# Kernel tuning notes

Hardware: AMD Instinct MI355X
Metric: run time of the kernel (lower is better)

The kernel has to match this reference:

```python
import jax, jax.numpy as jnp
import numpy as np

N_NODES = 40000
N_EDGES = 640000
D_FEAT = 128
HIDDEN = 128
N_GRAPHS = 512


def setup_inputs() -> dict:
    key = jax.random.key(0)
    ks = jax.random.split(key, 6)
    x = jax.random.normal(ks[0], (N_NODES, D_FEAT), dtype=jnp.float32)
    edge_index = jax.random.randint(ks[1], (2, N_EDGES), 0, N_NODES, dtype=jnp.int32)
    batch = jnp.sort(jax.random.randint(ks[2], (N_NODES,), 0, N_GRAPHS, dtype=jnp.int32))
    s1 = 1.0 / np.sqrt(D_FEAT)
    s2 = 1.0 / np.sqrt(HIDDEN)
    W1 = jax.random.normal(ks[3], (D_FEAT, HIDDEN), dtype=jnp.float32) * s1
    b1 = jnp.zeros((HIDDEN,), dtype=jnp.float32)
    W2 = jax.random.normal(ks[4], (HIDDEN, HIDDEN), dtype=jnp.float32) * s2
    b2 = jnp.zeros((HIDDEN,), dtype=jnp.float32)
    Wfc = jax.random.normal(ks[5], (HIDDEN, 1), dtype=jnp.float32) * s2
    bfc = jnp.zeros((1,), dtype=jnp.float32)
    return {"x": x, "edge_index": edge_index, "batch": batch,
            "W1": W1, "b1": b1, "W2": W2, "b2": b2, "Wfc": Wfc, "bfc": bfc}


def _gcn_conv(x, edge_index, W, b):
    # PyG GCNConv: linear transform, add self-loops, symmetric deg^{-1/2} norm,
    # scatter-add messages from row (source) to col (target), then bias.
    n = x.shape[0]
    h = x @ W  # [N, H]
    row, col = edge_index[0], edge_index[1]
    ones = jnp.ones_like(col, dtype=h.dtype)
    deg = 1.0 + jax.ops.segment_sum(ones, col, num_segments=n)  # self-loop included
    dinv = jax.lax.rsqrt(deg)  # [N]
    norm = dinv[row] * dinv[col]  # [E]
    msg = h[row] * norm[:, None]  # [E, H]
    out = jax.ops.segment_sum(msg, col, num_segments=n)
    out = out + h * (dinv * dinv)[:, None]  # self-loop contribution
    return out + b


def _mean_pool(x, batch, num_graphs):
    sums = jax.ops.segment_sum(x, batch, num_segments=num_graphs)
    cnt = jax.ops.segment_sum(jnp.ones((x.shape[0],), dtype=x.dtype), batch, num_segments=num_graphs)
    return sums / jnp.maximum(cnt, 1.0)[:, None]


def reference(x, edge_index, batch, W1, b1, W2, b2, Wfc, bfc):
    h = jax.nn.relu(_gcn_conv(x, edge_index, W1, b1))
    h = jax.nn.relu(_gcn_conv(h, edge_index, W2, b2))
    g = _mean_pool(h, batch, N_GRAPHS)  # [G, H]
    return g @ Wfc + bfc  # [G, 1]
```

## Files before the change

kernel.cpp:

```cpp
#include <hip/hip_runtime.h>
#include <hip/hip_fp16.h>

#define N_NODES 40000
#define N_EDGES 640000
#define NFEAT   128
#define N_GRAPHS 512
#define SCAN_NB 157
#define NBKT    157
#define BKT_CAP 8192
#define BIN_BLK_EDGES 2048
#define NBLK_A ((N_EDGES + BIN_BLK_EDGES - 1) / BIN_BLK_EDGES)
#define EPAD_MAX (N_EDGES + 3 * N_NODES)

__global__ void init_misc_kernel(int* __restrict__ gcursor, int* __restrict__ gcnt,
                                 float* __restrict__ out, const float* __restrict__ bfc,
                                 __half* __restrict__ hsent) {
    int t = threadIdx.x;
    if (t < NBKT) gcursor[t] = 0;
    float b = bfc[0];
    for (int i = t; i < N_GRAPHS; i += 256) { gcnt[i] = 0; out[i] = b; }
    if (t < NFEAT) hsent[t] = __float2half(0.0f);
}

__global__ void batch_hist_kernel(const int* __restrict__ batch, int* __restrict__ gcnt, int n) {
    int i = blockIdx.x * blockDim.x + threadIdx.x;
    if (i < n) atomicAdd(&gcnt[batch[i]], 1);
}

__global__ __launch_bounds__(256) void bin_kernel(const int* __restrict__ ei,
                                                  int* __restrict__ gcursor,
                                                  unsigned int* __restrict__ binned) {
    __shared__ int lhist[NBKT];
    __shared__ int lbase[NBKT];
    const int t  = threadIdx.x;
    const int e0 = blockIdx.x * BIN_BLK_EDGES;

    if (t < NBKT) lhist[t] = 0;
    __syncthreads();

    int creg[BIN_BLK_EDGES / 256];
    #pragma unroll
    for (int i = 0; i < BIN_BLK_EDGES / 256; ++i) {
        int e = e0 + i * 256 + t;
        creg[i] = (e < N_EDGES) ? ei[N_EDGES + e] : -1;
        if (creg[i] >= 0) atomicAdd(&lhist[creg[i] >> 8], 1);
    }
    __syncthreads();

    if (t < NBKT) { lbase[t] = atomicAdd(&gcursor[t], lhist[t]); lhist[t] = 0; }
    __syncthreads();

    #pragma unroll
    for (int i = 0; i < BIN_BLK_EDGES / 256; ++i) {
        int c = creg[i];
        if (c >= 0) {
            int e = e0 + i * 256 + t;
            int r = ei[e];
            int bkt = c >> 8;
            int slot = atomicAdd(&lhist[bkt], 1);
            binned[(size_t)bkt * BKT_CAP + lbase[bkt] + slot] =
                (unsigned int)r | ((unsigned int)(c & 255) << 16);
        }
    }
}

__global__ __launch_bounds__(256) void bucket_hist_kernel(const unsigned int* __restrict__ binned,
                                                          const int* __restrict__ gcursor,
                                                          float* __restrict__ dinv,
                                                          int* __restrict__ rowptr,
                                                          int* __restrict__ bsums) {
    __shared__ int chist[256];
    __shared__ int scn[256];
    const int b = blockIdx.x, t = threadIdx.x;
    chist[t] = 0;
    __syncthreads();
    const int cnt = gcursor[b];
    const unsigned int* src = binned + (size_t)b * BKT_CAP;
    for (int i = t; i < cnt; i += 256) atomicAdd(&chist[src[i] >> 16], 1);
    __syncthreads();
    const int col = b * 256 + t;
    const int valid = (col < N_NODES);
    int d = chist[t];
    if (valid) dinv[col] = rsqrtf(1.0f + (float)d);
    int pd = valid ? ((d + 3) & ~3) : 0;
    scn[t] = pd;
    __syncthreads();
    for (int off = 1; off < 256; off <<= 1) {
        int add = (t >= off) ? scn[t - off] : 0;
        __syncthreads();
        scn[t] += add;
        __syncthreads();
    }
    if (valid) rowptr[col] = scn[t] - pd;
    if (t == 255) bsums[b] = scn[255];
}

__global__ void scan157_kernel(int* __restrict__ bsums, int* __restrict__ rowptr) {
    __shared__ int tmp[256];
    int t = threadIdx.x;
    int v = (t < NBKT) ? bsums[t] : 0;
    tmp[t] = v;
    __syncthreads();
    for (int off = 1; off < 256; off <<= 1) {
        int add = (t >= off) ? tmp[t - off] : 0;
        __syncthreads();
        tmp[t] += add;
        __syncthreads();
    }
    if (t < NBKT) bsums[t] = tmp[t] - v;
    if (t == 255) rowptr[N_NODES] = tmp[255];
}

template <typename IdxT>
__global__ __launch_bounds__(256) void bucket_scatter_kernel(const unsigned int* __restrict__ binned,
                                                             const int* __restrict__ gcursor,
                                                             const int* __restrict__ bsums,
                                                             int* __restrict__ rowptr,
                                                             IdxT* __restrict__ csr) {
    __shared__ int ccur[256];
    const int b = blockIdx.x, t = threadIdx.x;
    const int col = b * 256 + t;
    const int base = bsums[b];
    int startp = 0;
    if (col < N_NODES) {
        startp = rowptr[col] + base;
        rowptr[col] = startp;
    }
    ccur[t] = startp;
    __syncthreads();
    const int cnt = gcursor[b];
    const unsigned int* src = binned + (size_t)b * BKT_CAP;
    for (int i = t; i < cnt; i += 256) {
        unsigned int u = src[i];
        int slot = atomicAdd(&ccur[u >> 16], 1);
        csr[slot] = (IdxT)(u & 0xFFFFu);
    }
    __syncthreads();
    if (col < N_NODES) {
        int cur = ccur[t];
        int deg = cur - startp;
        int endp = startp + ((deg + 3) & ~3);
        for (int p = cur; p < endp; ++p) csr[p] = (IdxT)N_NODES;
    }
}

__device__ inline float4 load_h4(const __half* p) {
    uint2 raw = *(const uint2*)p;
    __half2 h0 = *(__half2*)&raw.x;
    __half2 h1 = *(__half2*)&raw.y;
    float2 f0 = __half22float2(h0);
    float2 f1 = __half22float2(h1);
    return make_float4(f0.x, f0.y, f1.x, f1.y);
}
__device__ inline float4 load4v(const float* p)  { return *(const float4*)(p); }
__device__ inline float4 load4v(const __half* p) { return load_h4(p); }

template <typename InT>
__global__ __launch_bounds__(256, 4) void gemm64h_kernel(const InT* __restrict__ X,
                                                         const float* __restrict__ W,
                                                         const float* __restrict__ dinv,
                                                         __half* __restrict__ H) {
    __shared__ float Ws[128 * 64];
    const int colhalf = blockIdx.x & 1;
    const int tile    = blockIdx.x >> 1;

    for (int i = threadIdx.x; i < 2048; i += 256) {
        int k   = i >> 4;
        int cc4 = (i & 15) * 4;
        *(float4*)(Ws + k * 64 + cc4) = *(const float4*)(W + k * 128 + colhalf * 64 + cc4);
    }
    __syncthreads();

    const int rg = threadIdx.x >> 4;
    const int cg = threadIdx.x & 15;
    const int row0 = tile * 64 + rg * 4;
    const InT* x0 = X + (size_t)row0 * NFEAT;

    float acc[4][4] = {};
    float4 xc[4], xn[4];
    #pragma unroll
    for (int i = 0; i < 4; i++) xc[i] = load4v(x0 + (size_t)i * NFEAT);

    #pragma unroll 4
    for (int k = 0; k < 128; k += 4) {
        const int kn = (k + 4) & 127;
        #pragma unroll
        for (int i = 0; i < 4; i++) xn[i] = load4v(x0 + (size_t)i * NFEAT + kn);

        float4 wv[4];
        #pragma unroll
        for (int m = 0; m < 4; m++) wv[m] = *(const float4*)(Ws + (k + m) * 64 + cg * 4);

        #pragma unroll
        for (int i = 0; i < 4; i++) {
            const float xi[4] = {xc[i].x, xc[i].y, xc[i].z, xc[i].w};
            #pragma unroll
            for (int m = 0; m < 4; m++) {
                acc[i][0] += xi[m] * wv[m].x;
                acc[i][1] += xi[m] * wv[m].y;
                acc[i][2] += xi[m] * wv[m].z;
                acc[i][3] += xi[m] * wv[m].w;
            }
        }
        #pragma unroll
        for (int i = 0; i < 4; i++) xc[i] = xn[i];
    }

    #pragma unroll
    for (int i = 0; i < 4; i++) {
        float dr = dinv[row0 + i];
        __half2 p0 = __floats2half2_rn(acc[i][0] * dr, acc[i][1] * dr);
        __half2 p1 = __floats2half2_rn(acc[i][2] * dr, acc[i][3] * dr);
        uint2 pk;
        pk.x = *(unsigned int*)&p0;
        pk.y = *(unsigned int*)&p1;
        *(uint2*)(H + (size_t)(row0 + i) * NFEAT + colhalf * 64 + cg * 4) = pk;
    }
}

template <typename IdxT, typename IdxV, bool FUSE_POOL>
__global__ __launch_bounds__(256) void gather_h16_kernel(
        const int* __restrict__ rowptr, const IdxT* __restrict__ csr,
        const float* __restrict__ dinv, const __half* __restrict__ Ht,
        const float* __restrict__ bias, __half* __restrict__ outh,
        const float* __restrict__ Wfc, float* __restrict__ nodedot, int n) {
    int gid  = blockIdx.x * blockDim.x + threadIdx.x;
    int node = gid >> 6;
    if (node >= n) return;
    int lane = threadIdx.x & 63;
    int half = lane >> 5;
    int f4   = (lane & 31) * 4;

    int start = rowptr[node];
    int end   = rowptr[node + 1];

    float4 a0 = {0.f, 0.f, 0.f, 0.f};
    float4 a1 = {0.f, 0.f, 0.f, 0.f};
    if (half == 0) a0 = load_h4(Ht + (size_t)node * NFEAT + f4);

    IdxV nxt = *(const IdxV*)(csr + start);
    for (int j = start; j < end; j += 4) {
        IdxV cur = nxt;
        int jn = j + 4;
        if (jn < end) nxt = *(const IdxV*)(csr + jn);
        int r0 = half ? (int)cur.z : (int)cur.x;
        int r1 = half ? (int)cur.w : (int)cur.y;
        float4 v0 = load_h4(Ht + (size_t)r0 * NFEAT + f4);
        float4 v1 = load_h4(Ht + (size_t)r1 * NFEAT + f4);
        a0.x += v0.x; a0.y += v0.y; a0.z += v0.z; a0.w += v0.w;
        a1.x += v1.x; a1.y += v1.y; a1.z += v1.z; a1.w += v1.w;
    }
    a0.x += a1.x; a0.y += a1.y; a0.z += a1.z; a0.w += a1.w;

    a0.x += __shfl_xor(a0.x, 32, 64);
    a0.y += __shfl_xor(a0.y, 32, 64);
    a0.z += __shfl_xor(a0.z, 32, 64);
    a0.w += __shfl_xor(a0.w, 32, 64);

    if (half == 0) {
        float di  = dinv[node];
        float4 bb = *(const float4*)(bias + f4);
        float4 o;
        o.x = fmaxf(a0.x * di + bb.x, 0.0f);
        o.y = fmaxf(a0.y * di + bb.y, 0.0f);
        o.z = fmaxf(a0.z * di + bb.z, 0.0f);
        o.w = fmaxf(a0.w * di + bb.w, 0.0f);
        if (!FUSE_POOL) {
            __half2 p0 = __floats2half2_rn(o.x, o.y);
            __half2 p1 = __floats2half2_rn(o.z, o.w);
            uint2 pk;
            pk.x = *(unsigned int*)&p0;
            pk.y = *(unsigned int*)&p1;
            *(uint2*)(outh + (size_t)node * NFEAT + f4) = pk;
        } else {
            float4 wf = *(const float4*)(Wfc + f4);
            float d = o.x * wf.x + o.y * wf.y + o.z * wf.z + o.w * wf.w;
            d += __shfl_xor(d, 1, 64);
            d += __shfl_xor(d, 2, 64);
            d += __shfl_xor(d, 4, 64);
            d += __shfl_xor(d, 8, 64);
            d += __shfl_xor(d, 16, 64);
            if (lane == 0) nodedot[node] = d;
        }
    }
}

__global__ void pool_final_kernel(const float* __restrict__ nodedot,
                                  const int* __restrict__ batch,
                                  const int* __restrict__ gcnt,
                                  float* __restrict__ out, int n) {
    int i = blockIdx.x * blockDim.x + threadIdx.x;
    if (i < n) {
        int g = batch[i];
        int c = gcnt[g];
        float cf = (float)(c > 0 ? c : 1);
        atomicAdd(&out[g], nodedot[i] / cf);
    }
}

__global__ void edge_deg_int_kernel(const int* __restrict__ ei, int* __restrict__ degcnt, int E) {
    int e = blockIdx.x * blockDim.x + threadIdx.x;
    if (e < E) atomicAdd(&degcnt[ei[E + e]], 1);
}

__global__ void dinv_from_int_kernel(const int* __restrict__ degcnt, float* __restrict__ dinv, int n) {
    int i = blockIdx.x * blockDim.x + threadIdx.x;
    if (i < n) dinv[i] = rsqrtf(1.0f + (float)degcnt[i]);
}

__global__ __launch_bounds__(256, 4) void gemm64f_kernel(const float* __restrict__ X,
                                                         const float* __restrict__ W,
                                                         const float* __restrict__ dinv,
                                                         float* __restrict__ H) {
    __shared__ float Ws[128 * 64];
    const int colhalf = blockIdx.x & 1;
    const int tile    = blockIdx.x >> 1;
    for (int i = threadIdx.x; i < 2048; i += 256) {
        int k   = i >> 4;
        int cc4 = (i & 15) * 4;
        *(float4*)(Ws + k * 64 + cc4) = *(const float4*)(W + k * 128 + colhalf * 64 + cc4);
    }
    __syncthreads();
    const int rg = threadIdx.x >> 4;
    const int cg = threadIdx.x & 15;
    const int row0 = tile * 64 + rg * 4;
    const float* x0 = X + (size_t)row0 * NFEAT;
    float acc[4][4] = {};
    #pragma unroll 4
    for (int k = 0; k < 128; k += 4) {
        float4 xv[4];
        float4 wv[4];
        #pragma unroll
        for (int i = 0; i < 4; i++) xv[i] = *(const float4*)(x0 + (size_t)i * NFEAT + k);
        #pragma unroll
        for (int m = 0; m < 4; m++) wv[m] = *(const float4*)(Ws + (k + m) * 64 + cg * 4);
        #pragma unroll
        for (int i = 0; i < 4; i++) {
            const float xi[4] = {xv[i].x, xv[i].y, xv[i].z, xv[i].w};
            #pragma unroll
            for (int m = 0; m < 4; m++) {
                acc[i][0] += xi[m] * wv[m].x;
                acc[i][1] += xi[m] * wv[m].y;
                acc[i][2] += xi[m] * wv[m].z;
                acc[i][3] += xi[m] * wv[m].w;
            }
        }
    }
    #pragma unroll
    for (int i = 0; i < 4; i++) {
        float dr = dinv[row0 + i];
        float4 o = {acc[i][0] * dr, acc[i][1] * dr, acc[i][2] * dr, acc[i][3] * dr};
        *(float4*)(H + (size_t)(row0 + i) * NFEAT + cg * 4 + colhalf * 64) = o;
    }
}

__global__ __launch_bounds__(256) void edge_scatter_kernel(const int* __restrict__ ei,
                                                           const float* __restrict__ dinv,
                                                           const float* __restrict__ H,
                                                           float* __restrict__ agg,
                                                           int E) {
    long long gid = (long long)blockIdx.x * blockDim.x + threadIdx.x;
    int e = (int)(gid >> 5);
    if (e >= E) return;
    int c4 = ((int)gid & 31) * 4;
    int r = ei[e];
    int c = ei[E + e];
    float norm = dinv[c];
    const float4 hv = *(const float4*)(H + (size_t)r * NFEAT + c4);
    float* dst = agg + (size_t)c * NFEAT + c4;
    atomicAdd(dst + 0, hv.x * norm);
    atomicAdd(dst + 1, hv.y * norm);
    atomicAdd(dst + 2, hv.z * norm);
    atomicAdd(dst + 3, hv.w * norm);
}

__global__ void post_kernel(float* __restrict__ agg, const float* __restrict__ H,
                            const float* __restrict__ dinv, const float* __restrict__ b,
                            int n) {
    int gid = blockIdx.x * blockDim.x + threadIdx.x;
    if (gid >= n * 32) return;
    int node = gid >> 5;
    int c4 = (gid & 31) * 4;
    float s = dinv[node];
    float4 a  = *(float4*)(agg + (size_t)gid * 4);
    float4 hv = *(const float4*)(H + (size_t)gid * 4);
    float4 bb = *(const float4*)(b + c4);
    float4 o;
    o.x = fmaxf(a.x + hv.x * s + bb.x, 0.0f);
    o.y = fmaxf(a.y + hv.y * s + bb.y, 0.0f);
    o.z = fmaxf(a.z + hv.z * s + bb.z, 0.0f);
    o.w = fmaxf(a.w + hv.w * s + bb.w, 0.0f);
    *(float4*)(agg + (size_t)gid * 4) = o;
}

__global__ __launch_bounds__(128) void pool_fc_kernel(const float* __restrict__ H,
                                                      const int* __restrict__ batch,
                                                      const float* __restrict__ Wfc,
                                                      const float* __restrict__ bfc,
                                                      float* __restrict__ out, int n) {
    int g = blockIdx.x;
    int tid = threadIdx.x;
    int lo = 0, hi = n;
    while (lo < hi) { int mid = (lo + hi) >> 1; if (batch[mid] < g) lo = mid + 1; else hi = mid; }
    int start = lo;
    hi = n;
    while (lo < hi) { int mid = (lo + hi) >> 1; if (batch[mid] < g + 1) lo = mid + 1; else hi = mid; }
    int end = lo;
    float acc = 0.0f;
    for (int nd = start; nd < end; ++nd) acc += H[(size_t)nd * NFEAT + tid];
    float cnt = (float)((end - start) > 0 ? (end - start) : 1);
    float v = (acc / cnt) * Wfc[tid];
    __shared__ float red[128];
    red[tid] = v;
    __syncthreads();
    #pragma unroll
    for (int s = 64; s > 0; s >>= 1) {
        if (tid < s) red[tid] += red[tid + s];
        __syncthreads();
    }
    if (tid == 0) out[g] = red[0] + bfc[0];
}

static void run_csr_path(const float* x, const int* ei, const int* batch,
                         const float* W1, const float* b1, const float* W2,
                         const float* b2, const float* Wfc, const float* bfc,
                         float* out, void* d_ws, hipStream_t stream) {
    typedef unsigned short IdxT;
    typedef ushort4 IdxV;
    char* ws = (char*)d_ws;
    const size_t hbytes = (size_t)(N_NODES + 1) * NFEAT * sizeof(__half);
    const size_t obytes = (size_t)N_NODES * NFEAT * sizeof(__half);
    __half* hbuf  = (__half*)ws;
    __half* obuf  = (__half*)(ws + hbytes);
    IdxT*   csr   = (IdxT*)(ws + hbytes + obytes);
    char*   p     = ws + hbytes + obytes + ((size_t)EPAD_MAX * sizeof(IdxT) + 15) / 16 * 16;
    int*    rowptr = (int*)p;                p += ((size_t)(N_NODES + 1) * 4 + 15) / 16 * 16;
    float*  dinv   = (float*)p;              p += ((size_t)N_NODES * 4 + 15) / 16 * 16;
    int*    gcnt   = (int*)p;

    unsigned int* binned = (unsigned int*)obuf;
    int* bsums   = (int*)obuf + NBKT * BKT_CAP;
    int* gcursor = bsums + NBKT;
    float* nodedot = (float*)(p + (((size_t)N_GRAPHS * 4 + 15) / 16 * 16));

    init_misc_kernel<<<1, 256, 0, stream>>>(gcursor, gcnt, out, bfc,
                                            hbuf + (size_t)N_NODES * NFEAT);
    batch_hist_kernel<<<SCAN_NB, 256, 0, stream>>>(batch, gcnt, N_NODES);
    bin_kernel<<<NBLK_A, 256, 0, stream>>>(ei, gcursor, binned);
    bucket_hist_kernel<<<NBKT, 256, 0, stream>>>(binned, gcursor, dinv, rowptr, bsums);
    scan157_kernel<<<1, 256, 0, stream>>>(bsums, rowptr);
    bucket_scatter_kernel<IdxT><<<NBKT, 256, 0, stream>>>(binned, gcursor, bsums, rowptr, csr);

    gemm64h_kernel<float><<<(N_NODES / 64) * 2, 256, 0, stream>>>(x, W1, dinv, hbuf);
    gather_h16_kernel<IdxT, IdxV, false><<<(N_NODES * 64) / 256, 256, 0, stream>>>(
        rowptr, csr, dinv, hbuf, b1, obuf, nullptr, nullptr, N_NODES);

    gemm64h_kernel<__half><<<(N_NODES / 64) * 2, 256, 0, stream>>>(obuf, W2, dinv, hbuf);
    gather_h16_kernel<IdxT, IdxV, true><<<(N_NODES * 64) / 256, 256, 0, stream>>>(
        rowptr, csr, dinv, hbuf, b2, nullptr, Wfc, nodedot, N_NODES);

    pool_final_kernel<<<SCAN_NB, 256, 0, stream>>>(nodedot, batch, gcnt, out, N_NODES);
}

extern "C" void kernel_launch(void* const* d_in, const int* in_sizes, int n_in,
                              void* d_out, int out_size, void* d_ws, size_t ws_size,
                              hipStream_t stream) {
    const float* x     = (const float*)d_in[0];
    const int*   ei    = (const int*)  d_in[1];
    const int*   batch = (const int*)  d_in[2];
    const float* W1    = (const float*)d_in[3];
    const float* b1    = (const float*)d_in[4];
    const float* W2    = (const float*)d_in[5];
    const float* b2    = (const float*)d_in[6];
    const float* Wfc   = (const float*)d_in[7];
    const float* bfc   = (const float*)d_in[8];
    float* out = (float*)d_out;

    const size_t hbytes = (size_t)(N_NODES + 1) * NFEAT * sizeof(__half);
    const size_t obytes = (size_t)N_NODES * NFEAT * sizeof(__half);
    const size_t tail   = ((size_t)(N_NODES + 1) * 4 + 15) / 16 * 16
                        + ((size_t)N_NODES * 4 + 15) / 16 * 16
                        + (((size_t)N_GRAPHS * 4 + 15) / 16 * 16)
                        + (size_t)N_NODES * 4;
    const size_t need = hbytes + obytes + ((size_t)EPAD_MAX * 2 + 15) / 16 * 16 + tail;

    if (ws_size >= need) {
        run_csr_path(x, ei, batch, W1, b1, W2, b2, Wfc, bfc, out, d_ws, stream);
    } else {
        float* ws   = (float*)d_ws;
        int*   degc = (int*)ws;
        float* dinv = ws + N_NODES;
        float* hbuf = ws + 2 * N_NODES;
        float* agg  = hbuf + (size_t)N_NODES * NFEAT;
        const size_t fb2 = (size_t)N_NODES * NFEAT * sizeof(float);

        hipMemsetAsync(degc, 0, (size_t)N_NODES * sizeof(int), stream);
        edge_deg_int_kernel<<<N_EDGES / 256, 256, 0, stream>>>(ei, degc, N_EDGES);
        dinv_from_int_kernel<<<SCAN_NB, 256, 0, stream>>>(degc, dinv, N_NODES);

        hipMemsetAsync(agg, 0, fb2, stream);
        gemm64f_kernel<<<(N_NODES / 64) * 2, 256, 0, stream>>>(x, W1, dinv, hbuf);
        edge_scatter_kernel<<<(N_EDGES * 32) / 256, 256, 0, stream>>>(ei, dinv, hbuf, agg, N_EDGES);
        post_kernel<<<(N_NODES * 32) / 256, 256, 0, stream>>>(agg, hbuf, dinv, b1, N_NODES);

        gemm64f_kernel<<<(N_NODES / 64) * 2, 256, 0, stream>>>(agg, W2, dinv, hbuf);
        hipMemsetAsync(agg, 0, fb2, stream);
        edge_scatter_kernel<<<(N_EDGES * 32) / 256, 256, 0, stream>>>(ei, dinv, hbuf, agg, N_EDGES);
        post_kernel<<<(N_NODES * 32) / 256, 256, 0, stream>>>(agg, hbuf, dinv, b2, N_NODES);

        pool_fc_kernel<<<N_GRAPHS, 128, 0, stream>>>(agg, batch, Wfc, bfc, out, N_NODES);
    }
}
```

Baseline: 273.4 us.

## Fuse CSR build into one kernel and widen gather loads to 16 bytes

The three CSR-build kernels (bucket histogram, block-sum scan, bucket scatter) become one kernel. Each bucket claims its base offset with an atomic on a global counter, so bucket segments are placed in arrival order rather than in node order. Row start and padded length are packed into one rowptr word, which removes the rowptr[node+1] read and the separate scan pass. The gather kernel now processes four neighbors per wavefront step, with each lane loading 16 bytes (8 halves) instead of 8 bytes, and reduces the partial sums with two cross-lane shuffles. This trades two launches and some global traffic for a 20-bit packing limit on row starts and non-ordered CSR segments.

```diff
diff --git a/kernel.cpp b/kernel.cpp
--- a/kernel.cpp
+++ b/kernel.cpp
@@ -16,7 +16,7 @@
                                  float* __restrict__ out, const float* __restrict__ bfc,
                                  __half* __restrict__ hsent) {
     int t = threadIdx.x;
-    if (t < NBKT) gcursor[t] = 0;
+    if (t <= NBKT) gcursor[t] = 0;
     float b = bfc[0];
     for (int i = t; i < N_GRAPHS; i += 256) { gcnt[i] = 0; out[i] = b; }
     if (t < NFEAT) hsent[t] = __float2half(0.0f);
@@ -64,13 +64,17 @@
     }
 }
 
-__global__ __launch_bounds__(256) void bucket_hist_kernel(const unsigned int* __restrict__ binned,
-                                                          const int* __restrict__ gcursor,
-                                                          float* __restrict__ dinv,
-                                                          int* __restrict__ rowptr,
-                                                          int* __restrict__ bsums) {
+template <typename IdxT>
+__global__ __launch_bounds__(256) void bucket_build_kernel(const unsigned int* __restrict__ binned,
+                                                           const int* __restrict__ gcursor,
+                                                           int* __restrict__ gbase,
+                                                           float* __restrict__ dinv,
+                                                           int* __restrict__ rowptr,
+                                                           IdxT* __restrict__ csr) {
     __shared__ int chist[256];
     __shared__ int scn[256];
+    __shared__ int ccur[256];
+    __shared__ int sbase;
     const int b = blockIdx.x, t = threadIdx.x;
     chist[t] = 0;
     __syncthreads();
@@ -91,55 +95,21 @@
         scn[t] += add;
         __syncthreads();
     }
-    if (valid) rowptr[col] = scn[t] - pd;
-    if (t == 255) bsums[b] = scn[255];
-}
-
-__global__ void scan157_kernel(int* __restrict__ bsums, int* __restrict__ rowptr) {
-    __shared__ int tmp[256];
-    int t = threadIdx.x;
-    int v = (t < NBKT) ? bsums[t] : 0;
-    tmp[t] = v;
-    __syncthreads();
-    for (int off = 1; off < 256; off <<= 1) {
-        int add = (t >= off) ? tmp[t - off] : 0;
-        __syncthreads();
-        tmp[t] += add;
-        __syncthreads();
-    }
-    if (t < NBKT) bsums[t] = tmp[t] - v;
-    if (t == 255) rowptr[N_NODES] = tmp[255];
-}
-
-template <typename IdxT>
-__global__ __launch_bounds__(256) void bucket_scatter_kernel(const unsigned int* __restrict__ binned,
-                                                             const int* __restrict__ gcursor,
-                                                             const int* __restrict__ bsums,
-                                                             int* __restrict__ rowptr,
-                                                             IdxT* __restrict__ csr) {
-    __shared__ int ccur[256];
-    const int b = blockIdx.x, t = threadIdx.x;
-    const int col = b * 256 + t;
-    const int base = bsums[b];
-    int startp = 0;
-    if (col < N_NODES) {
-        startp = rowptr[col] + base;
-        rowptr[col] = startp;
-    }
-    ccur[t] = startp;
-    __syncthreads();
-    const int cnt = gcursor[b];
-    const unsigned int* src = binned + (size_t)b * BKT_CAP;
+    if (t == 255) sbase = atomicAdd(gbase, scn[255]);
+    __syncthreads();
+    const int start = sbase + scn[t] - pd;
+    if (valid) rowptr[col] = start | ((pd >> 2) << 20);
+    ccur[t] = start;
+    __syncthreads();
     for (int i = t; i < cnt; i += 256) {
         unsigned int u = src[i];
         int slot = atomicAdd(&ccur[u >> 16], 1);
         csr[slot] = (IdxT)(u & 0xFFFFu);
     }
     __syncthreads();
-    if (col < N_NODES) {
+    if (valid) {
         int cur = ccur[t];
-        int deg = cur - startp;
-        int endp = startp + ((deg + 3) & ~3);
+        int endp = start + pd;
         for (int p = cur; p < endp; ++p) csr[p] = (IdxT)N_NODES;
     }
 }
@@ -154,6 +124,14 @@
 }
 __device__ inline float4 load4v(const float* p)  { return *(const float4*)(p); }
 __device__ inline float4 load4v(const __half* p) { return load_h4(p); }
+
+__device__ inline void acc8(const uint4& raw, float* a) {
+    float2 f;
+    f = __half22float2(*(const __half2*)&raw.x); a[0] += f.x; a[1] += f.y;
+    f = __half22float2(*(const __half2*)&raw.y); a[2] += f.x; a[3] += f.y;
+    f = __half22float2(*(const __half2*)&raw.z); a[4] += f.x; a[5] += f.y;
+    f = __half22float2(*(const __half2*)&raw.w); a[6] += f.x; a[7] += f.y;
+}
 
 template <typename InT>
 __global__ __launch_bounds__(256, 4) void gemm64h_kernel(const InT* __restrict__ X,
@@ -219,7 +197,7 @@
 }
 
 template <typename IdxT, typename IdxV, bool FUSE_POOL>
-__global__ __launch_bounds__(256) void gather_h16_kernel(
+__global__ __launch_bounds__(256) void gather_w16_kernel(
         const int* __restrict__ rowptr, const IdxT* __restrict__ csr,
         const float* __restrict__ dinv, const __half* __restrict__ Ht,
         const float* __restrict__ bias, __half* __restrict__ outh,
@@ -228,60 +206,75 @@
     int node = gid >> 6;
     if (node >= n) return;
     int lane = threadIdx.x & 63;
-    int half = lane >> 5;
-    int f4   = (lane & 31) * 4;
-
-    int start = rowptr[node];
-    int end   = rowptr[node + 1];
-
-    float4 a0 = {0.f, 0.f, 0.f, 0.f};
-    float4 a1 = {0.f, 0.f, 0.f, 0.f};
-    if (half == 0) a0 = load_h4(Ht + (size_t)node * NFEAT + f4);
-
-    IdxV nxt = *(const IdxV*)(csr + start);
-    for (int j = start; j < end; j += 4) {
-        IdxV cur = nxt;
-        int jn = j + 4;
-        if (jn < end) nxt = *(const IdxV*)(csr + jn);
-        int r0 = half ? (int)cur.z : (int)cur.x;
-        int r1 = half ? (int)cur.w : (int)cur.y;
-        float4 v0 = load_h4(Ht + (size_t)r0 * NFEAT + f4);
-        float4 v1 = load_h4(Ht + (size_t)r1 * NFEAT + f4);
-        a0.x += v0.x; a0.y += v0.y; a0.z += v0.z; a0.w += v0.w;
-        a1.x += v1.x; a1.y += v1.y; a1.z += v1.z; a1.w += v1.w;
-    }
-    a0.x += a1.x; a0.y += a1.y; a0.z += a1.z; a0.w += a1.w;
-
-    a0.x += __shfl_xor(a0.x, 32, 64);
-    a0.y += __shfl_xor(a0.y, 32, 64);
-    a0.z += __shfl_xor(a0.z, 32, 64);
-    a0.w += __shfl_xor(a0.w, 32, 64);
-
-    if (half == 0) {
-        float di  = dinv[node];
-        float4 bb = *(const float4*)(bias + f4);
-        float4 o;
-        o.x = fmaxf(a0.x * di + bb.x, 0.0f);
-        o.y = fmaxf(a0.y * di + bb.y, 0.0f);
-        o.z = fmaxf(a0.z * di + bb.z, 0.0f);
-        o.w = fmaxf(a0.w * di + bb.w, 0.0f);
-        if (!FUSE_POOL) {
-            __half2 p0 = __floats2half2_rn(o.x, o.y);
-            __half2 p1 = __floats2half2_rn(o.z, o.w);
-            uint2 pk;
+    int q    = lane >> 4;
+    int fo   = lane & 15;
+
+    unsigned int u = (unsigned int)rowptr[node];
+    int start = (int)(u & 0xFFFFFu);
+    int pd    = (int)(u >> 20) << 2;
+    int end   = start + pd;
+
+    float a[8] = {0.f, 0.f, 0.f, 0.f, 0.f, 0.f, 0.f, 0.f};
+
+    if (q == 0) {
+        uint4 raw = *(const uint4*)(Ht + (size_t)node * NFEAT + fo * 8);
+        acc8(raw, a);
+    }
+
+    if (start < end) {
+        IdxV nxt = *(const IdxV*)(csr + start);
+        for (int j = start; j < end; j += 4) {
+            IdxV cur = nxt;
+            int jn = j + 4;
+            if (jn < end) nxt = *(const IdxV*)(csr + jn);
+            int r = (q == 0) ? (int)cur.x : (q == 1) ? (int)cur.y
+                  : (q == 2) ? (int)cur.z : (int)cur.w;
+            uint4 raw = *(const uint4*)(Ht + (size_t)r * NFEAT + fo * 8);
+            acc8(raw, a);
+        }
+    }
+
+    #pragma unroll
+    for (int i = 0; i < 8; i++) {
+        a[i] += __shfl_xor(a[i], 16, 64);
+        a[i] += __shfl_xor(a[i], 32, 64);
+    }
+
+    float di = dinv[node];
+    const float4 bb0 = *(const float4*)(bias + fo * 8);
+    const float4 bb1 = *(const float4*)(bias + fo * 8 + 4);
+    float o0 = fmaxf(a[0] * di + bb0.x, 0.0f);
+    float o1 = fmaxf(a[1] * di + bb0.y, 0.0f);
+    float o2 = fmaxf(a[2] * di + bb0.z, 0.0f);
+    float o3 = fmaxf(a[3] * di + bb0.w, 0.0f);
+    float o4 = fmaxf(a[4] * di + bb1.x, 0.0f);
+    float o5 = fmaxf(a[5] * di + bb1.y, 0.0f);
+    float o6 = fmaxf(a[6] * di + bb1.z, 0.0f);
+    float o7 = fmaxf(a[7] * di + bb1.w, 0.0f);
+
+    if (!FUSE_POOL) {
+        if (q == 0) {
+            __half2 p0 = __floats2half2_rn(o0, o1);
+            __half2 p1 = __floats2half2_rn(o2, o3);
+            __half2 p2 = __floats2half2_rn(o4, o5);
+            __half2 p3 = __floats2half2_rn(o6, o7);
+            uint4 pk;
             pk.x = *(unsigned int*)&p0;
             pk.y = *(unsigned int*)&p1;
-            *(uint2*)(outh + (size_t)node * NFEAT + f4) = pk;
-        } else {
-            float4 wf = *(const float4*)(Wfc + f4);
-            float d = o.x * wf.x + o.y * wf.y + o.z * wf.z + o.w * wf.w;
-            d += __shfl_xor(d, 1, 64);
-            d += __shfl_xor(d, 2, 64);
-            d += __shfl_xor(d, 4, 64);
-            d += __shfl_xor(d, 8, 64);
-            d += __shfl_xor(d, 16, 64);
-            if (lane == 0) nodedot[node] = d;
+            pk.z = *(unsigned int*)&p2;
+            pk.w = *(unsigned int*)&p3;
+            *(uint4*)(outh + (size_t)node * NFEAT + fo * 8) = pk;
         }
+    } else {
+        const float4 wf0 = *(const float4*)(Wfc + fo * 8);
+        const float4 wf1 = *(const float4*)(Wfc + fo * 8 + 4);
+        float dsum = o0 * wf0.x + o1 * wf0.y + o2 * wf0.z + o3 * wf0.w
+                   + o4 * wf1.x + o5 * wf1.y + o6 * wf1.z + o7 * wf1.w;
+        dsum += __shfl_xor(dsum, 1, 64);
+        dsum += __shfl_xor(dsum, 2, 64);
+        dsum += __shfl_xor(dsum, 4, 64);
+        dsum += __shfl_xor(dsum, 8, 64);
+        if (lane == 0) nodedot[node] = dsum;
     }
 }
 
@@ -439,24 +432,22 @@
     int*    gcnt   = (int*)p;
 
     unsigned int* binned = (unsigned int*)obuf;
-    int* bsums   = (int*)obuf + NBKT * BKT_CAP;
-    int* gcursor = bsums + NBKT;
+    int* gcursor = (int*)(binned + (size_t)NBKT * BKT_CAP);
     float* nodedot = (float*)(p + (((size_t)N_GRAPHS * 4 + 15) / 16 * 16));
 
     init_misc_kernel<<<1, 256, 0, stream>>>(gcursor, gcnt, out, bfc,
                                             hbuf + (size_t)N_NODES * NFEAT);
     batch_hist_kernel<<<SCAN_NB, 256, 0, stream>>>(batch, gcnt, N_NODES);
     bin_kernel<<<NBLK_A, 256, 0, stream>>>(ei, gcursor, binned);
-    bucket_hist_kernel<<<NBKT, 256, 0, stream>>>(binned, gcursor, dinv, rowptr, bsums);
-    scan157_kernel<<<1, 256, 0, stream>>>(bsums, rowptr);
-    bucket_scatter_kernel<IdxT><<<NBKT, 256, 0, stream>>>(binned, gcursor, bsums, rowptr, csr);
+    bucket_build_kernel<IdxT><<<NBKT, 256, 0, stream>>>(binned, gcursor, gcursor + NBKT,
+                                                        dinv, rowptr, csr);
 
     gemm64h_kernel<float><<<(N_NODES / 64) * 2, 256, 0, stream>>>(x, W1, dinv, hbuf);
-    gather_h16_kernel<IdxT, IdxV, false><<<(N_NODES * 64) / 256, 256, 0, stream>>>(
+    gather_w16_kernel<IdxT, IdxV, false><<<(N_NODES * 64) / 256, 256, 0, stream>>>(
         rowptr, csr, dinv, hbuf, b1, obuf, nullptr, nullptr, N_NODES);
 
     gemm64h_kernel<__half><<<(N_NODES / 64) * 2, 256, 0, stream>>>(obuf, W2, dinv, hbuf);
-    gather_h16_kernel<IdxT, IdxV, true><<<(N_NODES * 64) / 256, 256, 0, stream>>>(
+    gather_w16_kernel<IdxT, IdxV, true><<<(N_NODES * 64) / 256, 256, 0, stream>>>(
         rowptr, csr, dinv, hbuf, b2, nullptr, Wfc, nodedot, N_NODES);
 
     pool_final_kernel<<<SCAN_NB, 256, 0, stream>>>(nodedot, batch, gcnt, out, N_NODES);
```

After: 266.7 us, median of 2. -2.4%, faster.

## Fuse layer-1 gather with layer-2 GEMM and merge CSR build kernels

Applied to the files above, without the earlier changes.

Replaces the layer-1 aggregation kernel and the layer-2 GEMM with one kernel. Each block gathers 64 node rows into shared memory as half precision and multiplies them by W2 staged in shared memory, so the intermediate activations no longer go to global memory. It also merges the bucket histogram, the cross-bucket scan and the scatter into one kernel that takes its base offset with a global atomic. Row start and padded degree are packed into a single rowptr word. The changes remove two launches and one round trip of intermediate data, at the cost of a non-deterministic CSR ordering, a 20-bit limit on row offsets, and lower occupancy plus serialized per-wave gathers in the fused kernel.

```diff
diff --git a/kernel.cpp b/kernel.cpp
--- a/kernel.cpp
+++ b/kernel.cpp
@@ -14,12 +14,12 @@
 
 __global__ void init_misc_kernel(int* __restrict__ gcursor, int* __restrict__ gcnt,
                                  float* __restrict__ out, const float* __restrict__ bfc,
-                                 __half* __restrict__ hsent) {
+                                 __half* __restrict__ hsent1, __half* __restrict__ hsent2) {
     int t = threadIdx.x;
-    if (t < NBKT) gcursor[t] = 0;
+    if (t <= NBKT) gcursor[t] = 0;
     float b = bfc[0];
     for (int i = t; i < N_GRAPHS; i += 256) { gcnt[i] = 0; out[i] = b; }
-    if (t < NFEAT) hsent[t] = __float2half(0.0f);
+    if (t < NFEAT) { hsent1[t] = __float2half(0.0f); hsent2[t] = __float2half(0.0f); }
 }
 
 __global__ void batch_hist_kernel(const int* __restrict__ batch, int* __restrict__ gcnt, int n) {
@@ -64,13 +64,17 @@
     }
 }
 
-__global__ __launch_bounds__(256) void bucket_hist_kernel(const unsigned int* __restrict__ binned,
-                                                          const int* __restrict__ gcursor,
-                                                          float* __restrict__ dinv,
-                                                          int* __restrict__ rowptr,
-                                                          int* __restrict__ bsums) {
+template <typename IdxT>
+__global__ __launch_bounds__(256) void bucket_build_kernel(const unsigned int* __restrict__ binned,
+                                                           const int* __restrict__ gcursor,
+                                                           int* __restrict__ gbase,
+                                                           float* __restrict__ dinv,
+                                                           int* __restrict__ rowptr,
+                                                           IdxT* __restrict__ csr) {
     __shared__ int chist[256];
     __shared__ int scn[256];
+    __shared__ int ccur[256];
+    __shared__ int sbase;
     const int b = blockIdx.x, t = threadIdx.x;
     chist[t] = 0;
     __syncthreads();
@@ -91,55 +95,21 @@
         scn[t] += add;
         __syncthreads();
     }
-    if (valid) rowptr[col] = scn[t] - pd;
-    if (t == 255) bsums[b] = scn[255];
-}
-
-__global__ void scan157_kernel(int* __restrict__ bsums, int* __restrict__ rowptr) {
-    __shared__ int tmp[256];
-    int t = threadIdx.x;
-    int v = (t < NBKT) ? bsums[t] : 0;
-    tmp[t] = v;
-    __syncthreads();
-    for (int off = 1; off < 256; off <<= 1) {
-        int add = (t >= off) ? tmp[t - off] : 0;
-        __syncthreads();
-        tmp[t] += add;
-        __syncthreads();
-    }
-    if (t < NBKT) bsums[t] = tmp[t] - v;
-    if (t == 255) rowptr[N_NODES] = tmp[255];
-}
-
-template <typename IdxT>
-__global__ __launch_bounds__(256) void bucket_scatter_kernel(const unsigned int* __restrict__ binned,
-                                                             const int* __restrict__ gcursor,
-                                                             const int* __restrict__ bsums,
-                                                             int* __restrict__ rowptr,
-                                                             IdxT* __restrict__ csr) {
-    __shared__ int ccur[256];
-    const int b = blockIdx.x, t = threadIdx.x;
-    const int col = b * 256 + t;
-    const int base = bsums[b];
-    int startp = 0;
-    if (col < N_NODES) {
-        startp = rowptr[col] + base;
-        rowptr[col] = startp;
-    }
-    ccur[t] = startp;
-    __syncthreads();
-    const int cnt = gcursor[b];
-    const unsigned int* src = binned + (size_t)b * BKT_CAP;
+    if (t == 255) sbase = atomicAdd(gbase, scn[255]);
+    __syncthreads();
+    const int start = sbase + scn[t] - pd;
+    if (valid) rowptr[col] = start | ((pd >> 2) << 20);
+    ccur[t] = start;
+    __syncthreads();
     for (int i = t; i < cnt; i += 256) {
         unsigned int u = src[i];
         int slot = atomicAdd(&ccur[u >> 16], 1);
         csr[slot] = (IdxT)(u & 0xFFFFu);
     }
     __syncthreads();
-    if (col < N_NODES) {
+    if (valid) {
         int cur = ccur[t];
-        int deg = cur - startp;
-        int endp = startp + ((deg + 3) & ~3);
+        int endp = start + pd;
         for (int p = cur; p < endp; ++p) csr[p] = (IdxT)N_NODES;
     }
 }
@@ -215,6 +185,122 @@
         pk.x = *(unsigned int*)&p0;
         pk.y = *(unsigned int*)&p1;
         *(uint2*)(H + (size_t)(row0 + i) * NFEAT + colhalf * 64 + cg * 4) = pk;
+    }
+}
+
+template <typename IdxT, typename IdxV>
+__global__ __launch_bounds__(256, 3) void gather_gemm_kernel(
+        const int* __restrict__ rowptr, const IdxT* __restrict__ csr,
+        const float* __restrict__ dinv, const __half* __restrict__ Ht,
+        const float* __restrict__ bias, const float* __restrict__ W2,
+        __half* __restrict__ H2) {
+    __shared__ __half Xs[64][132];
+    __shared__ float Ws[128 * 64];
+    const int t    = threadIdx.x;
+    const int wv   = t >> 6;
+    const int lane = t & 63;
+    const int half = lane >> 5;
+    const int f4   = (lane & 31) * 4;
+    const int nbase = blockIdx.x * 64;
+
+    for (int i = t; i < 2048; i += 256) {
+        int k = i >> 4, cc4 = (i & 15) * 4;
+        *(float4*)(Ws + k * 64 + cc4) = *(const float4*)(W2 + k * 128 + cc4);
+    }
+
+    for (int i = 0; i < 16; ++i) {
+        const int nr   = wv * 16 + i;
+        const int node = nbase + nr;
+        unsigned int u = (unsigned int)rowptr[node];
+        int start = (int)(u & 0xFFFFFu);
+        int pd    = (int)(u >> 20) << 2;
+        int end   = start + pd;
+
+        float4 a0 = {0.f, 0.f, 0.f, 0.f};
+        float4 a1 = {0.f, 0.f, 0.f, 0.f};
+        if (half == 0) a0 = load_h4(Ht + (size_t)node * NFEAT + f4);
+
+        if (start < end) {
+            IdxV nxt = *(const IdxV*)(csr + start);
+            for (int j = start; j < end; j += 4) {
+                IdxV cur = nxt;
+                int jn = j + 4;
+                if (jn < end) nxt = *(const IdxV*)(csr + jn);
+                int r0 = half ? (int)cur.z : (int)cur.x;
+                int r1 = half ? (int)cur.w : (int)cur.y;
+                float4 v0 = load_h4(Ht + (size_t)r0 * NFEAT + f4);
+                float4 v1 = load_h4(Ht + (size_t)r1 * NFEAT + f4);
+                a0.x += v0.x; a0.y += v0.y; a0.z += v0.z; a0.w += v0.w;
+                a1.x += v1.x; a1.y += v1.y; a1.z += v1.z; a1.w += v1.w;
+            }
+        }
+        a0.x += a1.x; a0.y += a1.y; a0.z += a1.z; a0.w += a1.w;
+
+        a0.x += __shfl_xor(a0.x, 32, 64);
+        a0.y += __shfl_xor(a0.y, 32, 64);
+        a0.z += __shfl_xor(a0.z, 32, 64);
+        a0.w += __shfl_xor(a0.w, 32, 64);
+
+        if (half == 0) {
+            float di  = dinv[node];
+            float4 bb = *(const float4*)(bias + f4);
+            float o0 = fmaxf(a0.x * di + bb.x, 0.0f);
+            float o1 = fmaxf(a0.y * di + bb.y, 0.0f);
+            float o2 = fmaxf(a0.z * di + bb.z, 0.0f);
+            float o3 = fmaxf(a0.w * di + bb.w, 0.0f);
+            __half2 p0 = __floats2half2_rn(o0, o1);
+            __half2 p1 = __floats2half2_rn(o2, o3);
+            uint2 pk;
+            pk.x = *(unsigned int*)&p0;
+            pk.y = *(unsigned int*)&p1;
+            *(uint2*)&Xs[nr][f4] = pk;
+        }
+    }
+    __syncthreads();
+
+    const int rg  = t >> 4;
+    const int cg  = t & 15;
+    const int r0g = rg * 4;
+    #pragma unroll
+    for (int ch = 0; ch < 2; ++ch) {
+        if (ch == 1) {
+            __syncthreads();
+            for (int i = t; i < 2048; i += 256) {
+                int k = i >> 4, cc4 = (i & 15) * 4;
+                *(float4*)(Ws + k * 64 + cc4) = *(const float4*)(W2 + k * 128 + 64 + cc4);
+            }
+            __syncthreads();
+        }
+        float acc[4][4] = {};
+        #pragma unroll 4
+        for (int k = 0; k < 128; k += 4) {
+            float4 xv[4], wvv[4];
+            #pragma unroll
+            for (int i = 0; i < 4; i++) xv[i] = load_h4(&Xs[r0g + i][k]);
+            #pragma unroll
+            for (int m = 0; m < 4; m++) wvv[m] = *(const float4*)(Ws + (k + m) * 64 + cg * 4);
+            #pragma unroll
+            for (int i = 0; i < 4; i++) {
+                const float xi[4] = {xv[i].x, xv[i].y, xv[i].z, xv[i].w};
+                #pragma unroll
+                for (int m = 0; m < 4; m++) {
+                    acc[i][0] += xi[m] * wvv[m].x;
+                    acc[i][1] += xi[m] * wvv[m].y;
+                    acc[i][2] += xi[m] * wvv[m].z;
+                    acc[i][3] += xi[m] * wvv[m].w;
+                }
+            }
+        }
+        #pragma unroll
+        for (int i = 0; i < 4; i++) {
+            float dr = dinv[nbase + r0g + i];
+            __half2 p0 = __floats2half2_rn(acc[i][0] * dr, acc[i][1] * dr);
+            __half2 p1 = __floats2half2_rn(acc[i][2] * dr, acc[i][3] * dr);
+            uint2 pk;
+            pk.x = *(unsigned int*)&p0;
+            pk.y = *(unsigned int*)&p1;
+            *(uint2*)(H2 + (size_t)(nbase + r0g + i) * NFEAT + ch * 64 + cg * 4) = pk;
+        }
     }
 }
 
@@ -231,24 +317,28 @@
     int half = lane >> 5;
     int f4   = (lane & 31) * 4;
 
-    int start = rowptr[node];
-    int end   = rowptr[node + 1];
+    unsigned int u = (unsigned int)rowptr[node];
+    int start = (int)(u & 0xFFFFFu);
+    int pd    = (int)(u >> 20) << 2;
+    int end   = start + pd;
 
     float4 a0 = {0.f, 0.f, 0.f, 0.f};
     float4 a1 = {0.f, 0.f, 0.f, 0.f};
     if (half == 0) a0 = load_h4(Ht + (size_t)node * NFEAT + f4);
 
-    IdxV nxt = *(const IdxV*)(csr + start);
-    for (int j = start; j < end; j += 4) {
-        IdxV cur = nxt;
-        int jn = j + 4;
-        if (jn < end) nxt = *(const IdxV*)(csr + jn);
-        int r0 = half ? (int)cur.z : (int)cur.x;
-        int r1 = half ? (int)cur.w : (int)cur.y;
-        float4 v0 = load_h4(Ht + (size_t)r0 * NFEAT + f4);
-        float4 v1 = load_h4(Ht + (size_t)r1 * NFEAT + f4);
-        a0.x += v0.x; a0.y += v0.y; a0.z += v0.z; a0.w += v0.w;
-        a1.x += v1.x; a1.y += v1.y; a1.z += v1.z; a1.w += v1.w;
+    if (start < end) {
+        IdxV nxt = *(const IdxV*)(csr + start);
+        for (int j = start; j < end; j += 4) {
+            IdxV cur = nxt;
+            int jn = j + 4;
+            if (jn < end) nxt = *(const IdxV*)(csr + jn);
+            int r0 = half ? (int)cur.z : (int)cur.x;
+            int r1 = half ? (int)cur.w : (int)cur.y;
+            float4 v0 = load_h4(Ht + (size_t)r0 * NFEAT + f4);
+            float4 v1 = load_h4(Ht + (size_t)r1 * NFEAT + f4);
+            a0.x += v0.x; a0.y += v0.y; a0.z += v0.z; a0.w += v0.w;
+            a1.x += v1.x; a1.y += v1.y; a1.z += v1.z; a1.w += v1.w;
+        }
     }
     a0.x += a1.x; a0.y += a1.y; a0.z += a1.z; a0.w += a1.w;
 
@@ -429,36 +519,33 @@
     typedef ushort4 IdxV;
     char* ws = (char*)d_ws;
     const size_t hbytes = (size_t)(N_NODES + 1) * NFEAT * sizeof(__half);
-    const size_t obytes = (size_t)N_NODES * NFEAT * sizeof(__half);
     __half* hbuf  = (__half*)ws;
-    __half* obuf  = (__half*)(ws + hbytes);
-    IdxT*   csr   = (IdxT*)(ws + hbytes + obytes);
-    char*   p     = ws + hbytes + obytes + ((size_t)EPAD_MAX * sizeof(IdxT) + 15) / 16 * 16;
+    __half* hbuf2 = (__half*)(ws + hbytes);
+    IdxT*   csr   = (IdxT*)(ws + 2 * hbytes);
+    char*   p     = ws + 2 * hbytes + ((size_t)EPAD_MAX * sizeof(IdxT) + 15) / 16 * 16;
     int*    rowptr = (int*)p;                p += ((size_t)(N_NODES + 1) * 4 + 15) / 16 * 16;
     float*  dinv   = (float*)p;              p += ((size_t)N_NODES * 4 + 15) / 16 * 16;
     int*    gcnt   = (int*)p;
-
-    unsigned int* binned = (unsigned int*)obuf;
-    int* bsums   = (int*)obuf + NBKT * BKT_CAP;
-    int* gcursor = bsums + NBKT;
-    float* nodedot = (float*)(p + (((size_t)N_GRAPHS * 4 + 15) / 16 * 16));
+    float*  nodedot = (float*)(p + (((size_t)N_GRAPHS * 4 + 15) / 16 * 16));
+
+    unsigned int* binned = (unsigned int*)hbuf2;
+    int* gcursor = (int*)(binned + (size_t)NBKT * BKT_CAP);
 
     init_misc_kernel<<<1, 256, 0, stream>>>(gcursor, gcnt, out, bfc,
-                                            hbuf + (size_t)N_NODES * NFEAT);
+                                            hbuf  + (size_t)N_NODES * NFEAT,
+                                            hbuf2 + (size_t)N_NODES * NFEAT);
     batch_hist_kernel<<<SCAN_NB, 256, 0, stream>>>(batch, gcnt, N_NODES);
     bin_kernel<<<NBLK_A, 256, 0, stream>>>(ei, gcursor, binned);
-    bucket_hist_kernel<<<NBKT, 256, 0, stream>>>(binned, gcursor, dinv, rowptr, bsums);
-    scan157_kernel<<<1, 256, 0, stream>>>(bsums, rowptr);
-    bucket_scatter_kernel<IdxT><<<NBKT, 256, 0, stream>>>(binned, gcursor, bsums, rowptr, csr);
+    bucket_build_kernel<IdxT><<<NBKT, 256, 0, stream>>>(binned, gcursor, gcursor + NBKT,
+                                                        dinv, rowptr, csr);
 
     gemm64h_kernel<float><<<(N_NODES / 64) * 2, 256, 0, stream>>>(x, W1, dinv, hbuf);
-    gather_h16_kernel<IdxT, IdxV, false><<<(N_NODES * 64) / 256, 256, 0, stream>>>(
-        rowptr, csr, dinv, hbuf, b1, obuf, nullptr, nullptr, N_NODES);
-
-    gemm64h_kernel<__half><<<(N_NODES / 64) * 2, 256, 0, stream>>>(obuf, W2, dinv, hbuf);
+
+    gather_gemm_kernel<IdxT, IdxV><<<N_NODES / 64, 256, 0, stream>>>(
+        rowptr, csr, dinv, hbuf, b1, W2, hbuf2);
+
     gather_h16_kernel<IdxT, IdxV, true><<<(N_NODES * 64) / 256, 256, 0, stream>>>(
-        rowptr, csr, dinv, hbuf, b2, nullptr, Wfc, nodedot, N_NODES);
-
+        rowptr, csr, dinv, hbuf2, b2, nullptr, Wfc, nodedot, N_NODES);
     pool_final_kernel<<<SCAN_NB, 256, 0, stream>>>(nodedot, batch, gcnt, out, N_NODES);
 }
 
@@ -477,12 +564,11 @@
     float* out = (float*)d_out;
 
     const size_t hbytes = (size_t)(N_NODES + 1) * NFEAT * sizeof(__half);
-    const size_t obytes = (size_t)N_NODES * NFEAT * sizeof(__half);
     const size_t tail   = ((size_t)(N_NODES + 1) * 4 + 15) / 16 * 16
                         + ((size_t)N_NODES * 4 + 15) / 16 * 16
                         + (((size_t)N_GRAPHS * 4 + 15) / 16 * 16)
                         + (size_t)N_NODES * 4;
-    const size_t need = hbytes + obytes + ((size_t)EPAD_MAX * 2 + 15) / 16 * 16 + tail;
+    const size_t need = 2 * hbytes + ((size_t)EPAD_MAX * 2 + 15) / 16 * 16 + tail;
 
     if (ws_size >= need) {
         run_csr_path(x, ei, batch, W1, b1, W2, b2, Wfc, bfc, out, d_ws, stream);
```

New measurement: 290.2 us. +6.1%, slower.
